# Kernel tuning notes

Measured on AMD Instinct MI355X. Metric: run time of the kernel, lower is better.

## Reference

```python
import jax, jax.numpy as jnp
import numpy as np

DIM = 2048
N_HEADS = 32
N_KV_HEADS = 8
HEAD_DIM = DIM // N_HEADS
B, T = 2, 2048


def setup_inputs() -> dict:
    key = jax.random.key(0)
    ks = jax.random.split(key, 5)
    std = 0.02
    return {
        "x": jax.random.normal(ks[0], (B, T, DIM), dtype=jnp.float32),
        "wq": jax.random.normal(ks[1], (DIM, DIM), dtype=jnp.float32) * std,
        "wk": jax.random.normal(ks[2], (N_KV_HEADS * HEAD_DIM, DIM), dtype=jnp.float32) * std,
        "wv": jax.random.normal(ks[3], (N_KV_HEADS * HEAD_DIM, DIM), dtype=jnp.float32) * std,
        "wo": jax.random.normal(ks[4], (DIM, DIM), dtype=jnp.float32) * std,
    }


def _rope_tables(seq_len, head_dim, dtype):
    inv_freq = 1.0 / (10000.0 ** (jnp.arange(0, head_dim, 2, dtype=jnp.float32) / head_dim))
    t = jnp.arange(seq_len, dtype=jnp.float32)
    freqs = jnp.einsum("i,j->ij", t, inv_freq)          # [T, hd/2]
    emb = jnp.concatenate([freqs, freqs], axis=-1)       # [T, hd]
    return jnp.cos(emb).astype(dtype), jnp.sin(emb).astype(dtype)


def _rotate_half(x):
    h = x.shape[-1] // 2
    return jnp.concatenate([-x[..., h:], x[..., :h]], axis=-1)


def reference(x, wq, wk, wv, wo):
    Bc, Tc, C = x.shape
    q = (x @ wq.T).reshape(Bc, Tc, N_HEADS, HEAD_DIM).transpose(0, 2, 1, 3)      # [B,H,T,hd]
    k = (x @ wk.T).reshape(Bc, Tc, N_KV_HEADS, HEAD_DIM).transpose(0, 2, 1, 3)   # [B,Hk,T,hd]
    v = (x @ wv.T).reshape(Bc, Tc, N_KV_HEADS, HEAD_DIM).transpose(0, 2, 1, 3)

    cos, sin = _rope_tables(Tc, HEAD_DIM, x.dtype)  # [T,hd] broadcast over B,H
    q = q * cos + _rotate_half(q) * sin
    k = k * cos + _rotate_half(k) * sin

    rep = N_HEADS // N_KV_HEADS
    k = jnp.repeat(k, rep, axis=1)  # [B,H,T,hd]
    v = jnp.repeat(v, rep, axis=1)

    scale = 1.0 / np.sqrt(HEAD_DIM)
    scores = jnp.einsum("bhqd,bhkd->bhqk", q, k) * scale   # [B,H,T,T]
    causal = jnp.triu(jnp.ones((Tc, Tc), dtype=bool), k=1)
    scores = jnp.where(causal, jnp.asarray(-jnp.inf, scores.dtype), scores)
    attn = jax.nn.softmax(scores, axis=-1)
    out = jnp.einsum("bhqk,bhkd->bhqd", attn, v)           # [B,H,T,hd]
    out = out.transpose(0, 2, 1, 3).reshape(Bc, Tc, C)
    return out @ wo.T
```

## Files before the change

### kernel.cpp

```cpp
#include <hip/hip_runtime.h>


typedef unsigned short u16;
typedef __attribute__((ext_vector_type(8))) short bf16x8;
typedef __attribute__((ext_vector_type(4))) float f32x4;
typedef __attribute__((ext_vector_type(4))) unsigned short u16x4;

constexpr int T_SEQ = 2048;
constexpr int DIMC  = 2048;
constexpr int NHEAD = 32;
constexpr int HDIM  = 64;
constexpr int KVDIM = 512;
constexpr int BATCH = 2;

__device__ __forceinline__ u16 f2bf(float f) {
    union { float f; unsigned int i; } v; v.f = f;
    unsigned int r = v.i + 0x7FFFu + ((v.i >> 16) & 1u);
    return (u16)(r >> 16);
}

__device__ __forceinline__ unsigned int pack2_bf16(float e0, float e1) {
    return __builtin_amdgcn_perm(__float_as_uint(e1), __float_as_uint(e0),
                                 0x07060302u);
}

typedef __attribute__((address_space(1))) unsigned int as1_uint;
typedef __attribute__((address_space(3))) unsigned int as3_uint;
__device__ __forceinline__ void glds16(const u16* g, u16* l) {
    __builtin_amdgcn_global_load_lds((as1_uint*)(u16*)g, (as3_uint*)l, 16, 0, 0);
}

__global__ __launch_bounds__(256) void cvt5(const float* __restrict__ x,
                                            const float* __restrict__ wq,
                                            const float* __restrict__ wk,
                                            const float* __restrict__ wv,
                                            const float* __restrict__ wo,
                                            u16* __restrict__ xb,  u16* __restrict__ wqb,
                                            u16* __restrict__ wkb, u16* __restrict__ wvb,
                                            u16* __restrict__ wob) {
    constexpr int E0 = BATCH * T_SEQ * DIMC;
    constexpr int E1 = E0 + DIMC * DIMC;
    constexpr int E2 = E1 + KVDIM * DIMC;
    constexpr int E3 = E2 + KVDIM * DIMC;
    constexpr int E4 = E3 + DIMC * DIMC;
    for (int i = (blockIdx.x * 256 + threadIdx.x) * 4; i < E4; i += gridDim.x * 1024) {
        const float* s; u16* d; int off;
        if (i < E0)      { s = x;  d = xb;  off = 0;  }
        else if (i < E1) { s = wq; d = wqb; off = E0; }
        else if (i < E2) { s = wk; d = wkb; off = E1; }
        else if (i < E3) { s = wv; d = wvb; off = E2; }
        else             { s = wo; d = wob; off = E3; }
        f32x4 v = *(const f32x4*)(s + (i - off));
        u16x4 o;
        #pragma unroll
        for (int e = 0; e < 4; ++e) o[e] = f2bf(v[e]);
        *(u16x4*)(d + (i - off)) = o;
    }
}

template <bool OUTF32>
__device__ __forceinline__ void dgemm_core(const u16* __restrict__ A,
                                           const u16* __restrict__ W,
                                           void* __restrict__ Cv,
                                           int rowBase, int colBase,
                                           int N, int K, bool rope) {
    __shared__ __align__(16) u16 Ash[2][128 * 64];
    __shared__ __align__(16) u16 Bsh[2][128 * 64];

    const int tid  = threadIdx.x;
    const int lane = tid & 63;
    const int w    = tid >> 6;
    const int quad = lane >> 4;
    const int ln   = lane & 15;
    const int wm   = (w >> 1) * 64;
    const int wn   = (w & 1) * 64;

    const int sr = lane >> 3;
    const int sc = 8 * ((lane & 7) ^ sr);
    const u16* aS = A + (size_t)(rowBase + w * 8 + sr) * K + sc;
    const u16* bS = W + (size_t)(colBase + w * 8 + sr) * K + sc;

    f32x4 acc[4][4] = {};
    const int NT = K / 64;
    const int swz = (ln & 7) * 8;

    #pragma unroll
    for (int r = 0; r < 4; ++r) {
        glds16(aS + (size_t)(r * 32) * K, &Ash[0][(w + 4 * r) * 512]);
        glds16(bS + (size_t)(r * 32) * K, &Bsh[0][(w + 4 * r) * 512]);
    }

    for (int t = 0; t < NT; ++t) {
        const int cb = t & 1;
        __builtin_amdgcn_s_barrier();
        __builtin_amdgcn_sched_barrier(0);

        if (t + 1 < NT) {
            const size_t ko = (size_t)(t + 1) * 64;
            u16* An = &Ash[cb ^ 1][0];
            u16* Bn = &Bsh[cb ^ 1][0];
            #pragma unroll
            for (int r = 0; r < 4; ++r) {
                glds16(aS + ko + (size_t)(r * 32) * K, An + (w + 4 * r) * 512);
                glds16(bS + ko + (size_t)(r * 32) * K, Bn + (w + 4 * r) * 512);
            }
            __builtin_amdgcn_sched_barrier(0);
            __asm__ __volatile__("s_waitcnt vmcnt(8)" ::: "memory");
        } else {
            __asm__ __volatile__("s_waitcnt vmcnt(0)" ::: "memory");
        }
        __builtin_amdgcn_sched_barrier(0);
        __builtin_amdgcn_s_barrier();

        const u16* Ap = &Ash[cb][0];
        const u16* Bp = &Bsh[cb][0];
        #pragma unroll
        for (int q2 = 0; q2 < 2; ++q2) {
            bf16x8 bwf[4];
            #pragma unroll
            for (int n = 0; n < 4; ++n)
                bwf[n] = *(const bf16x8*)(Bp + (wn + n * 16 + ln) * 64
                                             + ((q2 * 32 + quad * 8) ^ swz));
            __builtin_amdgcn_s_setprio(1);
            #pragma unroll
            for (int m = 0; m < 4; ++m) {
                bf16x8 af = *(const bf16x8*)(Ap + (wm + m * 16 + ln) * 64
                                                + ((q2 * 32 + quad * 8) ^ swz));
                #pragma unroll
                for (int n = 0; n < 4; ++n)
                    acc[m][n] = __builtin_amdgcn_mfma_f32_16x16x32_bf16(af, bwf[n], acc[m][n], 0, 0, 0);
            }
            __builtin_amdgcn_s_setprio(0);
        }
    }

    if (rope) {
        #pragma unroll
        for (int j = 0; j < 2; ++j) {
            const int d = j * 16 + ln;
            const float invrev = exp2f(-(float)d * (13.287712379549449f / 32.0f))
                                 * 0.15915494309189535f;
            #pragma unroll
            for (int i = 0; i < 4; ++i) {
                #pragma unroll
                for (int r = 0; r < 4; ++r) {
                    const int t = (rowBase + wm + i * 16 + quad * 4 + r) & (T_SEQ - 1);
                    float rev = (float)t * invrev;
                    float fr = rev - floorf(rev);
                    float sn = __builtin_amdgcn_sinf(fr);
                    float cs = __builtin_amdgcn_cosf(fr);
                    float a0 = acc[i][j][r], a2 = acc[i][j + 2][r];
                    acc[i][j][r]     = a0 * cs - a2 * sn;
                    acc[i][j + 2][r] = a2 * cs + a0 * sn;
                }
            }
        }
    }

    #pragma unroll
    for (int i = 0; i < 4; ++i) {
        int mrow = rowBase + wm + i * 16 + quad * 4;
        #pragma unroll
        for (int j = 0; j < 4; ++j) {
            int n = colBase + wn + j * 16 + ln;
            #pragma unroll
            for (int r = 0; r < 4; ++r) {
                if constexpr (OUTF32)
                    ((float*)Cv)[(size_t)(mrow + r) * N + n] = acc[i][j][r];
                else
                    ((u16*)Cv)[(size_t)(mrow + r) * N + n] = f2bf(acc[i][j][r]);
            }
        }
    }
}

__global__ __launch_bounds__(256, 2) void qkv_gemm(const u16* __restrict__ xb,
                                                   const u16* __restrict__ wqb,
                                                   const u16* __restrict__ wkb,
                                                   const u16* __restrict__ wvb,
                                                   u16* __restrict__ Qb,
                                                   u16* __restrict__ Kb,
                                                   u16* __restrict__ Vb) {
    const int flat = blockIdx.y * 24 + blockIdx.x;
    const int xcd  = flat & 7;
    const int idx  = flat >> 3;
    const int row  = (xcd >> 2) * 16 + idx / 6;
    const int ct   = (xcd & 3) * 6 + idx % 6;
    const int rowBase = row * 128;

    const u16* W; u16* C; int colBase, N; bool rope;
    if (ct < 16)      { W = wqb; C = Qb; colBase = ct * 128;        N = DIMC;  rope = true; }
    else if (ct < 20) { W = wkb; C = Kb; colBase = (ct - 16) * 128; N = KVDIM; rope = true; }
    else              { W = wvb; C = Vb; colBase = (ct - 20) * 128; N = KVDIM; rope = false; }
    dgemm_core<false>(xb, W, C, rowBase, colBase, N, DIMC, rope);
}

__global__ __launch_bounds__(256, 2) void gemm_out(const u16* __restrict__ A,
                                                   const u16* __restrict__ W,
                                                   float* __restrict__ C) {
    const int flat = blockIdx.y * 16 + blockIdx.x;
    const int xcd  = flat & 7;
    const int idx  = flat >> 3;
    const int row  = (xcd >> 2) * 16 + (idx >> 2);
    const int col  = (xcd & 3) * 4 + (idx & 3);
    dgemm_core<true>(A, W, C, row * 128, col * 128, DIMC, DIMC, false);
}

__global__ __launch_bounds__(256) void transpose_v(const u16* __restrict__ V,
                                                   u16* __restrict__ Vt) {
    __shared__ __align__(16) u16 tile[32][33];
    const int x = threadIdx.x & 31;
    const int y = threadIdx.x >> 5;
    const int tok0 = blockIdx.y * 32;
    const int c0   = blockIdx.x * 32;
    #pragma unroll
    for (int yy = 0; yy < 32; yy += 8)
        tile[y + yy][x] = V[(size_t)(tok0 + y + yy) * KVDIM + c0 + x];
    __syncthreads();
    const int b  = tok0 >> 11;
    const int t0 = tok0 & (T_SEQ - 1);
    #pragma unroll
    for (int yy = 0; yy < 32; yy += 8)
        Vt[(size_t)(b * KVDIM + c0 + y + yy) * T_SEQ + t0 + x] = tile[x][y + yy];
}

__global__ __launch_bounds__(256) void attn(const u16* __restrict__ Q,
                                            const u16* __restrict__ Kx,
                                            const u16* __restrict__ Vt,
                                            u16* __restrict__ O) {
    __shared__ __align__(16) u16 Ks[2][64][72];
    __shared__ __align__(16) u16 Vs[2][64][72];

    const int tid  = threadIdx.x;
    const int lane = tid & 63;
    const int w    = tid >> 6;
    const int quad = lane >> 4;
    const int ln   = lane & 15;
    const int h    = blockIdx.y;
    const int b    = blockIdx.z;
    const int kvh  = h >> 2;

    const int srow = tid >> 2;
    const int c    = tid & 3;
    const int scol = c * 16;
    const int vsb  = 32 * (c >> 1) + 4 * (c & 1);
    const u16* kbase = Kx + (size_t)(b * T_SEQ + srow) * KVDIM + kvh * HDIM + scol;
    const u16* vbase = Vt + (size_t)(b * KVDIM + kvh * HDIM + srow) * T_SEQ;

    const float K1 = 0.125f * 1.4426950408889634f;
    const float K2 = 8.0f * 1.4426950408889634f;

    #pragma unroll
    for (int phase = 0; phase < 2; ++phase) {
        const int qt = phase ? (31 - (int)blockIdx.x) : (int)blockIdx.x;
        const int qr0 = qt * 64 + w * 16;

        const u16* qp = Q + (size_t)(b * T_SEQ + qr0 + ln) * DIMC + h * HDIM + quad * 8;
        const bf16x8 bq0 = *(const bf16x8*)qp;
        const bf16x8 bq1 = *(const bf16x8*)(qp + 32);

        f32x4 o[4] = {};
        float lsum = 0.0f;

        bf16x8 kra = *(const bf16x8*)kbase;
        bf16x8 krb = *(const bf16x8*)(kbase + 8);
        bf16x8 vra = *(const bf16x8*)(vbase + scol);
        bf16x8 vrb = *(const bf16x8*)(vbase + scol + 8);

        for (int kt = 0; kt <= qt; ++kt) {
            const int cb = kt & 1;

            *(bf16x8*)&Ks[cb][srow][scol]     = kra;
            *(bf16x8*)&Ks[cb][srow][scol + 8] = krb;
            {
                union { bf16x8 v; u16x4 h4[2]; } ua, ub;
                ua.v = vra; ub.v = vrb;
                *(u16x4*)&Vs[cb][srow][vsb]      = ua.h4[0];
                *(u16x4*)&Vs[cb][srow][vsb + 8]  = ua.h4[1];
                *(u16x4*)&Vs[cb][srow][vsb + 16] = ub.h4[0];
                *(u16x4*)&Vs[cb][srow][vsb + 24] = ub.h4[1];
            }

            if (kt < qt) {
                const size_t ko = (size_t)(kt + 1) * 64;
                kra = *(const bf16x8*)(kbase + ko * KVDIM);
                krb = *(const bf16x8*)(kbase + ko * KVDIM + 8);
                vra = *(const bf16x8*)(vbase + ko + scol);
                vrb = *(const bf16x8*)(vbase + ko + scol + 8);
            }

            __asm__ __volatile__("s_waitcnt lgkmcnt(0)" ::: "memory");
            __builtin_amdgcn_s_barrier();

            f32x4 s[4];
            __builtin_amdgcn_s_setprio(1);
            #pragma unroll
            for (int st = 0; st < 4; ++st) {
                f32x4 z = {};
                s[st] = __builtin_amdgcn_mfma_f32_16x16x32_bf16(
                            *(const bf16x8*)&Ks[cb][st * 16 + ln][quad * 8], bq0, z, 0, 0, 0);
                s[st] = __builtin_amdgcn_mfma_f32_16x16x32_bf16(
                            *(const bf16x8*)&Ks[cb][st * 16 + ln][32 + quad * 8], bq1, s[st], 0, 0, 0);
            }
            __builtin_amdgcn_s_setprio(0);

            unsigned int pk[8];
            if (kt != qt) {
                #pragma unroll
                for (int st = 0; st < 4; ++st) {
                    float e0 = exp2f(fmaf(s[st][0], K1, -K2));
                    float e1 = exp2f(fmaf(s[st][1], K1, -K2));
                    float e2 = exp2f(fmaf(s[st][2], K1, -K2));
                    float e3 = exp2f(fmaf(s[st][3], K1, -K2));
                    lsum += (e0 + e1) + (e2 + e3);
                    pk[2 * st]     = pack2_bf16(e0, e1);
                    pk[2 * st + 1] = pack2_bf16(e2, e3);
                }
            } else {
                const int thr = w * 16 + ln;
                #pragma unroll
                for (int st = 0; st < 4; ++st) {
                    float e[4];
                    #pragma unroll
                    for (int r = 0; r < 4; ++r) {
                        const int key = st * 16 + quad * 4 + r;
                        e[r] = (key > thr) ? 0.0f : exp2f(fmaf(s[st][r], K1, -K2));
                    }
                    lsum += (e[0] + e[1]) + (e[2] + e[3]);
                    pk[2 * st]     = pack2_bf16(e[0], e[1]);
                    pk[2 * st + 1] = pack2_bf16(e[2], e[3]);
                }
            }

            union { unsigned int u[4]; bf16x8 v; } a0, a1;
            a0.u[0] = pk[0]; a0.u[1] = pk[1]; a0.u[2] = pk[2]; a0.u[3] = pk[3];
            a1.u[0] = pk[4]; a1.u[1] = pk[5]; a1.u[2] = pk[6]; a1.u[3] = pk[7];

            __builtin_amdgcn_s_setprio(1);
            #pragma unroll
            for (int t = 0; t < 4; ++t) {
                o[t] = __builtin_amdgcn_mfma_f32_16x16x32_bf16(
                           a0.v, *(const bf16x8*)&Vs[cb][t * 16 + ln][quad * 8], o[t], 0, 0, 0);
                o[t] = __builtin_amdgcn_mfma_f32_16x16x32_bf16(
                           a1.v, *(const bf16x8*)&Vs[cb][t * 16 + ln][32 + quad * 8], o[t], 0, 0, 0);
            }
            __builtin_amdgcn_s_setprio(0);
        }

        float ls = lsum;
        ls += __shfl_xor(ls, 16);
        ls += __shfl_xor(ls, 32);
        #pragma unroll
        for (int r = 0; r < 4; ++r) {
            const float inv = 1.0f / __shfl(ls, quad * 4 + r);
            size_t obase = (size_t)(b * T_SEQ + qr0 + quad * 4 + r) * DIMC + h * HDIM;
            #pragma unroll
            for (int t = 0; t < 4; ++t)
                O[obase + t * 16 + ln] = f2bf(o[t][r] * inv);
        }

        __syncthreads();
    }
}

extern "C" void kernel_launch(void* const* d_in, const int* in_sizes, int n_in,
                              void* d_out, int out_size, void* d_ws, size_t ws_size,
                              hipStream_t stream) {
    const float* x  = (const float*)d_in[0];
    const float* wq = (const float*)d_in[1];
    const float* wk = (const float*)d_in[2];
    const float* wv = (const float*)d_in[3];
    const float* wo = (const float*)d_in[4];
    float* out = (float*)d_out;

    char* ws = (char*)d_ws;
    constexpr size_t MB = 1024 * 1024;
    u16* Qb  = (u16*)(ws);
    u16* Kb  = (u16*)(ws + 16 * MB);
    u16* Vb  = (u16*)(ws + 20 * MB);
    u16* Vtb = (u16*)(ws + 24 * MB);
    u16* AOb = (u16*)(ws + 28 * MB);
    u16* xb  = AOb;
    u16* wqb = (u16*)(ws + 44 * MB);
    u16* wkb = (u16*)(ws + 52 * MB);
    u16* wvb = (u16*)(ws + 54 * MB);
    u16* wob = (u16*)(ws + 56 * MB);
    const int M = BATCH * T_SEQ;

    hipLaunchKernelGGL(cvt5, dim3(2048), dim3(256), 0, stream,
                       x, wq, wk, wv, wo, xb, wqb, wkb, wvb, wob);
    hipLaunchKernelGGL(qkv_gemm, dim3(24, M / 128), dim3(256), 0, stream,
                       xb, wqb, wkb, wvb, Qb, Kb, Vb);
    hipLaunchKernelGGL(transpose_v, dim3(KVDIM / 32, M / 32), dim3(256), 0, stream, Vb, Vtb);
    hipLaunchKernelGGL(attn, dim3(16, NHEAD, BATCH), dim3(256), 0, stream,
                       Qb, Kb, Vtb, AOb);
    hipLaunchKernelGGL(gemm_out, dim3(DIMC / 128, M / 128), dim3(256), 0, stream,
                       AOb, wob, out);
}
```

Baseline: 288.2 us.

## Process two 64-row query tiles per block to reuse K/V tiles

Each attention block now handles 128 query rows (two 64-row groups per warp) instead of 64, so every K/V tile staged in shared memory feeds twice as many MFMAs and the K/V global loads per query are halved. The grid shrinks from 16 to 8 blocks along the query axis, and the causal-mask logic is generalized to handle the diagonal for each sub-tile. This raises register pressure (double accumulators and Q fragments), may lower occupancy, and wastes some compute on the partially masked extra key tile. With fewer blocks (512 total) the balance across CUs may also change.

Measured after the change: 288.9 us. No clear change (+0.2%).

```diff
diff --git a/kernel.cpp b/kernel.cpp
--- a/kernel.cpp
+++ b/kernel.cpp
@@ -252,22 +252,26 @@
 
     #pragma unroll
     for (int phase = 0; phase < 2; ++phase) {
-        const int qt = phase ? (31 - (int)blockIdx.x) : (int)blockIdx.x;
-        const int qr0 = qt * 64 + w * 16;
-
-        const u16* qp = Q + (size_t)(b * T_SEQ + qr0 + ln) * DIMC + h * HDIM + quad * 8;
-        const bf16x8 bq0 = *(const bf16x8*)qp;
-        const bf16x8 bq1 = *(const bf16x8*)(qp + 32);
-
-        f32x4 o[4] = {};
-        float lsum = 0.0f;
+        const int qt = phase ? (15 - (int)blockIdx.x) : (int)blockIdx.x;
+        const int qr0 = qt * 128 + w * 16;
+
+        const u16* qp0 = Q + (size_t)(b * T_SEQ + qr0 + ln) * DIMC + h * HDIM + quad * 8;
+        const u16* qp1 = qp0 + (size_t)64 * DIMC;
+        const bf16x8 bq00 = *(const bf16x8*)qp0;
+        const bf16x8 bq01 = *(const bf16x8*)(qp0 + 32);
+        const bf16x8 bq10 = *(const bf16x8*)qp1;
+        const bf16x8 bq11 = *(const bf16x8*)(qp1 + 32);
+
+        f32x4 o0[4] = {}, o1[4] = {};
+        float ls0 = 0.0f, ls1 = 0.0f;
 
         bf16x8 kra = *(const bf16x8*)kbase;
         bf16x8 krb = *(const bf16x8*)(kbase + 8);
         bf16x8 vra = *(const bf16x8*)(vbase + scol);
         bf16x8 vrb = *(const bf16x8*)(vbase + scol + 8);
 
-        for (int kt = 0; kt <= qt; ++kt) {
+        const int NTk = 2 * qt + 2;
+        for (int kt = 0; kt < NTk; ++kt) {
             const int cb = kt & 1;
 
             *(bf16x8*)&Ks[cb][srow][scol]     = kra;
@@ -281,7 +285,7 @@
                 *(u16x4*)&Vs[cb][srow][vsb + 24] = ub.h4[1];
             }
 
-            if (kt < qt) {
+            if (kt + 1 < NTk) {
                 const size_t ko = (size_t)(kt + 1) * 64;
                 kra = *(const bf16x8*)(kbase + ko * KVDIM);
                 krb = *(const bf16x8*)(kbase + ko * KVDIM + 8);
@@ -292,71 +296,90 @@
             __asm__ __volatile__("s_waitcnt lgkmcnt(0)" ::: "memory");
             __builtin_amdgcn_s_barrier();
 
-            f32x4 s[4];
+            f32x4 s0[4], s1[4];
             __builtin_amdgcn_s_setprio(1);
             #pragma unroll
             for (int st = 0; st < 4; ++st) {
-                f32x4 z = {};
-                s[st] = __builtin_amdgcn_mfma_f32_16x16x32_bf16(
-                            *(const bf16x8*)&Ks[cb][st * 16 + ln][quad * 8], bq0, z, 0, 0, 0);
-                s[st] = __builtin_amdgcn_mfma_f32_16x16x32_bf16(
-                            *(const bf16x8*)&Ks[cb][st * 16 + ln][32 + quad * 8], bq1, s[st], 0, 0, 0);
+                bf16x8 kfa = *(const bf16x8*)&Ks[cb][st * 16 + ln][quad * 8];
+                bf16x8 kfb = *(const bf16x8*)&Ks[cb][st * 16 + ln][32 + quad * 8];
+                f32x4 z0 = {}, z1 = {};
+                s0[st] = __builtin_amdgcn_mfma_f32_16x16x32_bf16(kfa, bq00, z0, 0, 0, 0);
+                s1[st] = __builtin_amdgcn_mfma_f32_16x16x32_bf16(kfa, bq10, z1, 0, 0, 0);
+                s0[st] = __builtin_amdgcn_mfma_f32_16x16x32_bf16(kfb, bq01, s0[st], 0, 0, 0);
+                s1[st] = __builtin_amdgcn_mfma_f32_16x16x32_bf16(kfb, bq11, s1[st], 0, 0, 0);
             }
             __builtin_amdgcn_s_setprio(0);
 
-            unsigned int pk[8];
-            if (kt != qt) {
+            unsigned int pk0[8], pk1[8];
+            #pragma unroll
+            for (int g = 0; g < 2; ++g) {
+                const f32x4* s = g ? s1 : s0;
+                unsigned int* pk = g ? pk1 : pk0;
+                float lsum = 0.0f;
+                const int kdiff = kt - (2 * qt + g);
+                if (kdiff < 0) {
+                    #pragma unroll
+                    for (int st = 0; st < 4; ++st) {
+                        float e0 = exp2f(fmaf(s[st][0], K1, -K2));
+                        float e1 = exp2f(fmaf(s[st][1], K1, -K2));
+                        float e2 = exp2f(fmaf(s[st][2], K1, -K2));
+                        float e3 = exp2f(fmaf(s[st][3], K1, -K2));
+                        lsum += (e0 + e1) + (e2 + e3);
+                        pk[2 * st]     = pack2_bf16(e0, e1);
+                        pk[2 * st + 1] = pack2_bf16(e2, e3);
+                    }
+                } else {
+                    const int thr = w * 16 + ln - 64 * kdiff;
+                    #pragma unroll
+                    for (int st = 0; st < 4; ++st) {
+                        float e[4];
+                        #pragma unroll
+                        for (int r = 0; r < 4; ++r) {
+                            const int key = st * 16 + quad * 4 + r;
+                            e[r] = (key > thr) ? 0.0f : exp2f(fmaf(s[st][r], K1, -K2));
+                        }
+                        lsum += (e[0] + e[1]) + (e[2] + e[3]);
+                        pk[2 * st]     = pack2_bf16(e[0], e[1]);
+                        pk[2 * st + 1] = pack2_bf16(e[2], e[3]);
+                    }
+                }
+                if (g) ls1 += lsum; else ls0 += lsum;
+            }
+
+            union { unsigned int u[4]; bf16x8 v; } a00, a01, a10, a11;
+            a00.u[0] = pk0[0]; a00.u[1] = pk0[1]; a00.u[2] = pk0[2]; a00.u[3] = pk0[3];
+            a01.u[0] = pk0[4]; a01.u[1] = pk0[5]; a01.u[2] = pk0[6]; a01.u[3] = pk0[7];
+            a10.u[0] = pk1[0]; a10.u[1] = pk1[1]; a10.u[2] = pk1[2]; a10.u[3] = pk1[3];
+            a11.u[0] = pk1[4]; a11.u[1] = pk1[5]; a11.u[2] = pk1[6]; a11.u[3] = pk1[7];
+
+            __builtin_amdgcn_s_setprio(1);
+            #pragma unroll
+            for (int t = 0; t < 4; ++t) {
+                bf16x8 vfa = *(const bf16x8*)&Vs[cb][t * 16 + ln][quad * 8];
+                bf16x8 vfb = *(const bf16x8*)&Vs[cb][t * 16 + ln][32 + quad * 8];
+                o0[t] = __builtin_amdgcn_mfma_f32_16x16x32_bf16(a00.v, vfa, o0[t], 0, 0, 0);
+                o1[t] = __builtin_amdgcn_mfma_f32_16x16x32_bf16(a10.v, vfa, o1[t], 0, 0, 0);
+                o0[t] = __builtin_amdgcn_mfma_f32_16x16x32_bf16(a01.v, vfb, o0[t], 0, 0, 0);
+                o1[t] = __builtin_amdgcn_mfma_f32_16x16x32_bf16(a11.v, vfb, o1[t], 0, 0, 0);
+            }
+            __builtin_amdgcn_s_setprio(0);
+        }
+
+        #pragma unroll
+        for (int g = 0; g < 2; ++g) {
+            float ls = g ? ls1 : ls0;
+            const f32x4* o = g ? o1 : o0;
+            ls += __shfl_xor(ls, 16);
+            ls += __shfl_xor(ls, 32);
+            #pragma unroll
+            for (int r = 0; r < 4; ++r) {
+                const float inv = 1.0f / __shfl(ls, quad * 4 + r);
+                size_t obase = (size_t)(b * T_SEQ + qr0 + g * 64 + quad * 4 + r) * DIMC
+                               + h * HDIM;
                 #pragma unroll
-                for (int st = 0; st < 4; ++st) {
-                    float e0 = exp2f(fmaf(s[st][0], K1, -K2));
-                    float e1 = exp2f(fmaf(s[st][1], K1, -K2));
-                    float e2 = exp2f(fmaf(s[st][2], K1, -K2));
-                    float e3 = exp2f(fmaf(s[st][3], K1, -K2));
-                    lsum += (e0 + e1) + (e2 + e3);
-                    pk[2 * st]     = pack2_bf16(e0, e1);
-                    pk[2 * st + 1] = pack2_bf16(e2, e3);
-                }
-            } else {
-                const int thr = w * 16 + ln;
-                #pragma unroll
-                for (int st = 0; st < 4; ++st) {
-                    float e[4];
-                    #pragma unroll
-                    for (int r = 0; r < 4; ++r) {
-                        const int key = st * 16 + quad * 4 + r;
-                        e[r] = (key > thr) ? 0.0f : exp2f(fmaf(s[st][r], K1, -K2));
-                    }
-                    lsum += (e[0] + e[1]) + (e[2] + e[3]);
-                    pk[2 * st]     = pack2_bf16(e[0], e[1]);
-                    pk[2 * st + 1] = pack2_bf16(e[2], e[3]);
-                }
-            }
-
-            union { unsigned int u[4]; bf16x8 v; } a0, a1;
-            a0.u[0] = pk[0]; a0.u[1] = pk[1]; a0.u[2] = pk[2]; a0.u[3] = pk[3];
-            a1.u[0] = pk[4]; a1.u[1] = pk[5]; a1.u[2] = pk[6]; a1.u[3] = pk[7];
-
-            __builtin_amdgcn_s_setprio(1);
-            #pragma unroll
-            for (int t = 0; t < 4; ++t) {
-                o[t] = __builtin_amdgcn_mfma_f32_16x16x32_bf16(
-                           a0.v, *(const bf16x8*)&Vs[cb][t * 16 + ln][quad * 8], o[t], 0, 0, 0);
-                o[t] = __builtin_amdgcn_mfma_f32_16x16x32_bf16(
-                           a1.v, *(const bf16x8*)&Vs[cb][t * 16 + ln][32 + quad * 8], o[t], 0, 0, 0);
-            }
-            __builtin_amdgcn_s_setprio(0);
-        }
-
-        float ls = lsum;
-        ls += __shfl_xor(ls, 16);
-        ls += __shfl_xor(ls, 32);
-        #pragma unroll
-        for (int r = 0; r < 4; ++r) {
-            const float inv = 1.0f / __shfl(ls, quad * 4 + r);
-            size_t obase = (size_t)(b * T_SEQ + qr0 + quad * 4 + r) * DIMC + h * HDIM;
-            #pragma unroll
-            for (int t = 0; t < 4; ++t)
-                O[obase + t * 16 + ln] = f2bf(o[t][r] * inv);
+                for (int t = 0; t < 4; ++t)
+                    O[obase + t * 16 + ln] = f2bf(o[t][r] * inv);
+            }
         }
 
         __syncthreads();
@@ -392,7 +415,7 @@
     hipLaunchKernelGGL(qkv_gemm, dim3(24, M / 128), dim3(256), 0, stream,
                        xb, wqb, wkb, wvb, Qb, Kb, Vb);
     hipLaunchKernelGGL(transpose_v, dim3(KVDIM / 32, M / 32), dim3(256), 0, stream, Vb, Vtb);
-    hipLaunchKernelGGL(attn, dim3(16, NHEAD, BATCH), dim3(256), 0, stream,
+    hipLaunchKernelGGL(attn, dim3(8, NHEAD, BATCH), dim3(256), 0, stream,
                        Qb, Kb, Vtb, AOb);
     hipLaunchKernelGGL(gemm_out, dim3(DIMC / 128, M / 128), dim3(256), 0, stream,
                        AOb, wob, out);
```
